# Performance work log

Hardware: AMD Instinct MI355X
Metric: run time of the kernel (lower is better)

## Reference

```python
import jax, jax.numpy as jnp
import numpy as np

B, C, H, W, N = 256, 64, 36, 36, 2000
P = H * W  # 1296 mask pixels


def setup_inputs() -> dict:
    key = jax.random.key(0)
    k1, k2, k3 = jax.random.split(key, 3)
    x = jax.random.normal(k1, (B, C, H, W), dtype=jnp.float32)
    # init_scales rows 1 and 2 give (mean=0, std=0.01) for both param tensors
    mask_weights = 0.01 * jax.random.normal(k2, (P, C, N), dtype=jnp.float32)
    readout_weights = 0.01 * jax.random.normal(k3, (C, N), dtype=jnp.float32)
    return {"x": x, "mask_weights": mask_weights, "readout_weights": readout_weights}


def reference(x, mask_weights, readout_weights):
    # x: (B, C, H, W) -> flatten spatial dims to P
    b, c, h, w = x.shape
    x_flat = x.reshape(b, c, h * w)  # (B, C, P)
    # Per-channel spatial pooling fused with weighted channel sum:
    # masked[b,c,n] = sum_p x_flat[b,c,p] * mask_weights[p,c,n]
    # out[b,n]     = sum_c masked[b,c,n] * readout_weights[c,n]
    out = jnp.einsum("bcp,pcn,cn->bn", x_flat, mask_weights, readout_weights)
    # final_relu=False => no bias / softplus
    return out
```

## Files before the change

kernel.cpp:

```cpp
#include <hip/hip_runtime.h>

typedef unsigned short ushort_t;
typedef unsigned int uint_t;
typedef __attribute__((ext_vector_type(8))) short bf16x8;
typedef __attribute__((ext_vector_type(4))) float f32x4;

#define C_DIM 64
#define P_DIM 1296
#define N_DIM 2000
#define B_DIM 256
#define K_DIM (C_DIM * P_DIM)
#define XB_ELEMS (B_DIM * K_DIM)
#define XB_ELEMS_PAD (XB_ELEMS + 256)
#define XB_BYTES ((size_t)XB_ELEMS_PAD * 2)
#define SLICES 32
#define OUT_ELEMS (B_DIM * N_DIM)
#define NSTEP 42

static __device__ __forceinline__ ushort_t f2bf(float f) {
  unsigned u = __builtin_bit_cast(unsigned, f);
  u += 0x7fffu + ((u >> 16) & 1u);
  return (ushort_t)(u >> 16);
}

__global__ void klindt_cvt_kernel(const float4* __restrict__ x,
                                  unsigned long long* __restrict__ xb) {
  int idx = blockIdx.x * 256 + threadIdx.x;
  if (idx >= XB_ELEMS_PAD / 4) return;
  unsigned long long r = 0ull;
  if (idx < XB_ELEMS / 4) {
    float4 v = x[idx];
    r = (unsigned long long)f2bf(v.x) | ((unsigned long long)f2bf(v.y) << 16) |
        ((unsigned long long)f2bf(v.z) << 32) |
        ((unsigned long long)f2bf(v.w) << 48);
  }
  xb[idx] = r;
}

__global__ void __launch_bounds__(512, 4) klindt_gemm_kernel(
    const char* __restrict__ xbb, const char* __restrict__ mwb,
    const float* __restrict__ rw, float* __restrict__ partials) {
  __shared__ ushort_t sA[2][16384];

  const int tid = threadIdx.x;
  const int lane = tid & 63;
  const int wid = tid >> 6;
  const int r15 = lane & 15, g4 = lane >> 4;
  const int bid = blockIdx.x;
  const int slice = (bid & 7) + 8 * ((bid >> 3) & 3);
  const int n0 = (bid >> 5) * 128;
  const int c0 = slice * 2;

  f32x4 acc[16];
#pragma unroll
  for (int i = 0; i < 16; ++i) {
    acc[i][0] = 0.f; acc[i][1] = 0.f; acc[i][2] = 0.f; acc[i][3] = 0.f;
  }

  uint_t a_gbase[4]; int a_doff[4];
#pragma unroll
  for (int it = 0; it < 4; ++it) {
    int chunk = it * 512 + tid;
    int row = chunk >> 3, sl = chunk & 7;
    int ss = sl ^ (row & 7);
    a_gbase[it] = (uint_t)(row * K_DIM + ss * 8) * 2u;
    a_doff[it] = chunk * 8;
  }

  const int nidx = n0 + wid * 16 + r15;
  const bool okn = nidx < N_DIM;
  const uint_t nb4 = (uint_t)(okn ? nidx : (N_DIM - 1)) * 4u;
  const float rvl = okn ? rw[c0 * N_DIM + nidx] : 0.f;
  const float rvh = okn ? rw[(c0 + 1) * N_DIM + nidx] : 0.f;
  const uint_t pg = (uint_t)(g4 * 8);

  const int swz7 = r15 & 7;
  const int aoff0 = r15 * 128 + ((g4 ^ swz7) & 7) * 16;
  const int aoff1 = r15 * 128 + (((g4 + 4) ^ swz7) & 7) * 16;

  float mvE[16], mvO[16];

  auto issueA = [&](int buf, int t) {
    int half = (t >= 21) ? 1 : 0;
    int sp = t - 21 * half;
    uint_t kb = ((uint_t)(c0 + half) * (uint_t)P_DIM + (uint_t)sp * 64u) * 2u;
#pragma unroll
    for (int it = 0; it < 4; ++it) {
      const char* g = xbb + (a_gbase[it] + kb);
      __builtin_amdgcn_global_load_lds(
          (const __attribute__((address_space(1))) unsigned int*)g,
          (__attribute__((address_space(3))) unsigned int*)(&sA[buf][a_doff[it]]),
          16, 0, 0);
    }
  };

#define ISSUE_B(MV, T)                                                        \
  do {                                                                        \
    int half_ = ((T) >= 21) ? 1 : 0;                                          \
    int sp_ = (T)-21 * half_;                                                 \
    uint_t pa_ = (uint_t)(sp_ * 64) + pg;                                     \
    uint_t pb_ = pa_ + 32u;                                                   \
    if (pa_ > 1288u) pa_ = 1288u;       \
    if (pb_ > 1288u) pb_ = 1288u;                                             \
    uint_t cb_ = (uint_t)(c0 + half_) * 8000u + nb4;                          \
    const char* ba_ = mwb + (pa_ * 512000u + cb_);                            \
    const char* bb_ = mwb + (pb_ * 512000u + cb_);                            \
    _Pragma("unroll") for (int j_ = 0; j_ < 8; ++j_)                          \
        MV[j_] = *(const float*)(ba_ + (uint_t)j_ * 512000u);                 \
    _Pragma("unroll") for (int j_ = 0; j_ < 8; ++j_)                          \
        MV[8 + j_] = *(const float*)(bb_ + (uint_t)j_ * 512000u);             \
  } while (0)

#define CVT_COMPUTE(BUF, MV, T)                                               \
  do {                                                                        \
    int half_ = ((T) >= 21) ? 1 : 0;                                          \
    int sp_ = (T)-21 * half_;                                                 \
    float rv_ = half_ ? rvh : rvl;                                            \
    float rva_ = (sp_ < 20 || g4 < 2) ? rv_ : 0.f;                            \
    float rvb_ = (sp_ < 20) ? rv_ : 0.f;                                      \
    bf16x8 b0_, b1_;                                                          \
    _Pragma("unroll") for (int j_ = 0; j_ < 8; ++j_) {                        \
      b0_[j_] = (short)f2bf(MV[j_] * rva_);                                   \
      b1_[j_] = (short)f2bf(MV[8 + j_] * rvb_);                               \
    }                                                                         \
    __builtin_amdgcn_s_setprio(1);                                            \
    _Pragma("unroll") for (int fm_ = 0; fm_ < 16; ++fm_) {                    \
      bf16x8 a0_ = *(const bf16x8*)((const char*)&sA[BUF][0] +                \
                                    (aoff0 + fm_ * 2048));                    \
      acc[fm_] = __builtin_amdgcn_mfma_f32_16x16x32_bf16(a0_, b0_, acc[fm_],  \
                                                         0, 0, 0);            \
      bf16x8 a1_ = *(const bf16x8*)((const char*)&sA[BUF][0] +                \
                                    (aoff1 + fm_ * 2048));                    \
      acc[fm_] = __builtin_amdgcn_mfma_f32_16x16x32_bf16(a1_, b1_, acc[fm_],  \
                                                         0, 0, 0);            \
    }                                                                         \
    __builtin_amdgcn_s_setprio(0);                                            \
  } while (0)

  issueA(0, 0);
  ISSUE_B(mvE, 0);
  asm volatile("s_waitcnt vmcnt(16) lgkmcnt(0)" ::: "memory");
  __builtin_amdgcn_sched_barrier(0);
  __builtin_amdgcn_s_barrier();
  __builtin_amdgcn_sched_barrier(0);

#define BODY(S, MV_CUR, MV_NEXT)                                              \
  {                                                                           \
    issueA(((S) + 1) & 1, (S) + 1);            \
    ISSUE_B(MV_NEXT, (S) + 1);             \
    CVT_COMPUTE((S)&1, MV_CUR, S);        \
    asm volatile("s_waitcnt vmcnt(16) lgkmcnt(0)" ::: "memory");              \
    __builtin_amdgcn_sched_barrier(0);                                        \
    __builtin_amdgcn_s_barrier();                                             \
    __builtin_amdgcn_sched_barrier(0);                                        \
  }

  for (int s = 0; s < 40; s += 2) {
    BODY(s, mvE, mvO);
    BODY(s + 1, mvO, mvE);
  }
  BODY(40, mvE, mvO);
  CVT_COMPUTE(1, mvO, 41);

  float* pb = partials + (size_t)slice * OUT_ELEMS;
  if (okn) {
#pragma unroll
    for (int fm = 0; fm < 16; ++fm) {
#pragma unroll
      for (int rr = 0; rr < 4; ++rr) {
        int m = fm * 16 + g4 * 4 + rr;
        pb[m * N_DIM + nidx] = acc[fm][rr];
      }
    }
  }
#undef BODY
#undef ISSUE_B
#undef CVT_COMPUTE
}

__global__ void klindt_reduce_kernel(const float* __restrict__ part,
                                     float* __restrict__ out) {
  int i = blockIdx.x * 256 + threadIdx.x;
  if (i < OUT_ELEMS) {
    float s = 0.f;
#pragma unroll
    for (int k = 0; k < SLICES; ++k) s += part[(size_t)k * OUT_ELEMS + i];
    out[i] = s;
  }
}

extern "C" void kernel_launch(void* const* d_in, const int* in_sizes, int n_in,
                              void* d_out, int out_size, void* d_ws,
                              size_t ws_size, hipStream_t stream) {
  (void)in_sizes; (void)n_in; (void)out_size; (void)ws_size;
  const float* x = (const float*)d_in[0];
  const char* mwb = (const char*)d_in[1];
  const float* rw = (const float*)d_in[2];
  float* out = (float*)d_out;

  char* xbb = (char*)d_ws;
  float* partials = (float*)((char*)d_ws + XB_BYTES);

  {
    int nvec = XB_ELEMS_PAD / 4;
    int grid = (nvec + 255) / 256;
    klindt_cvt_kernel<<<grid, 256, 0, stream>>>((const float4*)x,
                                                (unsigned long long*)xbb);
  }
  {
    klindt_gemm_kernel<<<512, 512, 0, stream>>>(xbb, mwb, rw, partials);
  }
  {
    int grid = (OUT_ELEMS + 255) / 256;
    klindt_reduce_kernel<<<grid, 256, 0, stream>>>(partials, out);
  }
}
```

Baseline: 244.8 us.

## Retile GEMM to per-wave private LDS buffers with 128x32 wave tiles, no block barriers

The GEMM kernel changes from 512-thread blocks covering all 256 batch rows and 128 outputs to 256-thread blocks covering 128 rows. Each wave stages its own A tile in a private LDS region and computes a 128x32 output tile. This drops the block-wide s_barrier per K step and halves A reuse across waves, so each wave issues 16 LDS-direct loads per step. The aim is to remove block synchronization stalls and raise occupancy. The cost is more redundant A traffic from global/L2 and single-buffered staging within each wave.

```diff
diff --git a/kernel.cpp b/kernel.cpp
--- a/kernel.cpp
+++ b/kernel.cpp
@@ -15,7 +15,6 @@
 #define XB_BYTES ((size_t)XB_ELEMS_PAD * 2)
 #define SLICES 32
 #define OUT_ELEMS (B_DIM * N_DIM)
-#define NSTEP 42
 
 static __device__ __forceinline__ ushort_t f2bf(float f) {
   unsigned u = __builtin_bit_cast(unsigned, f);
@@ -37,10 +36,10 @@
   xb[idx] = r;
 }
 
-__global__ void __launch_bounds__(512, 4) klindt_gemm_kernel(
+__global__ void __launch_bounds__(256, 2) klindt_gemm_kernel(
     const char* __restrict__ xbb, const char* __restrict__ mwb,
     const float* __restrict__ rw, float* __restrict__ partials) {
-  __shared__ ushort_t sA[2][16384];
+  __shared__ ushort_t sA[4][8192];
 
   const int tid = threadIdx.x;
   const int lane = tid & 63;
@@ -48,134 +47,149 @@
   const int r15 = lane & 15, g4 = lane >> 4;
   const int bid = blockIdx.x;
   const int slice = (bid & 7) + 8 * ((bid >> 3) & 3);
-  const int n0 = (bid >> 5) * 128;
+  const int r5 = bid >> 5;
+  const int m0 = (r5 & 1) * 128;
+  const int nb = ((r5 >> 1) * 4 + wid) * 32;
   const int c0 = slice * 2;
 
-  f32x4 acc[16];
-#pragma unroll
-  for (int i = 0; i < 16; ++i) {
-    acc[i][0] = 0.f; acc[i][1] = 0.f; acc[i][2] = 0.f; acc[i][3] = 0.f;
-  }
-
-  uint_t a_gbase[4]; int a_doff[4];
-#pragma unroll
-  for (int it = 0; it < 4; ++it) {
-    int chunk = it * 512 + tid;
-    int row = chunk >> 3, sl = chunk & 7;
-    int ss = sl ^ (row & 7);
-    a_gbase[it] = (uint_t)(row * K_DIM + ss * 8) * 2u;
-    a_doff[it] = chunk * 8;
-  }
-
-  const int nidx = n0 + wid * 16 + r15;
-  const bool okn = nidx < N_DIM;
-  const uint_t nb4 = (uint_t)(okn ? nidx : (N_DIM - 1)) * 4u;
-  const float rvl = okn ? rw[c0 * N_DIM + nidx] : 0.f;
-  const float rvh = okn ? rw[(c0 + 1) * N_DIM + nidx] : 0.f;
+  ushort_t* myA = sA[wid];
+
+  f32x4 acc[8][2];
+#pragma unroll
+  for (int i = 0; i < 8; ++i)
+#pragma unroll
+    for (int j = 0; j < 2; ++j) {
+      acc[i][j][0] = 0.f; acc[i][j][1] = 0.f;
+      acc[i][j][2] = 0.f; acc[i][j][3] = 0.f;
+    }
+
+  const int ss8 = (((lane & 7) ^ ((lane >> 3) & 7))) * 8;
+  const uint_t a_srcm = (uint_t)(m0 + (lane >> 3)) * (uint_t)K_DIM * 2u;
+
+  const int nA = nb + r15, nB = nb + 16 + r15;
+  const bool okA = nA < N_DIM, okB = nB < N_DIM;
+  const uint_t nAb = (uint_t)(okA ? nA : N_DIM - 1) * 4u;
+  const uint_t nBb = (uint_t)(okB ? nB : N_DIM - 1) * 4u;
+  const float rv0l = okA ? rw[c0 * N_DIM + nA] : 0.f;
+  const float rv1l = okB ? rw[c0 * N_DIM + nB] : 0.f;
+  const float rv0h = okA ? rw[(c0 + 1) * N_DIM + nA] : 0.f;
+  const float rv1h = okB ? rw[(c0 + 1) * N_DIM + nB] : 0.f;
   const uint_t pg = (uint_t)(g4 * 8);
 
-  const int swz7 = r15 & 7;
-  const int aoff0 = r15 * 128 + ((g4 ^ swz7) & 7) * 16;
-  const int aoff1 = r15 * 128 + (((g4 + 4) ^ swz7) & 7) * 16;
+  const int aoff0 = r15 * 128 + ((g4 ^ (r15 & 7)) & 7) * 16;
+  const int aoff1 = r15 * 128 + (((g4 + 4) ^ (r15 & 7)) & 7) * 16;
 
   float mvE[16], mvO[16];
-
-  auto issueA = [&](int buf, int t) {
-    int half = (t >= 21) ? 1 : 0;
-    int sp = t - 21 * half;
-    uint_t kb = ((uint_t)(c0 + half) * (uint_t)P_DIM + (uint_t)sp * 64u) * 2u;
-#pragma unroll
-    for (int it = 0; it < 4; ++it) {
-      const char* g = xbb + (a_gbase[it] + kb);
-      __builtin_amdgcn_global_load_lds(
-          (const __attribute__((address_space(1))) unsigned int*)g,
-          (__attribute__((address_space(3))) unsigned int*)(&sA[buf][a_doff[it]]),
-          16, 0, 0);
+  bf16x8 bf0, bf1;
+
+#define STAGE(C, P0)                                                          \
+  do {                                                                        \
+    uint_t kl_ = (uint_t)(P0) + (uint_t)ss8;                                  \
+    if (kl_ > 1288u) kl_ = 1288u;                \
+    uint_t ko_ = ((uint_t)(C) * (uint_t)P_DIM + kl_) * 2u;                    \
+    const char* s_ = xbb + (a_srcm + ko_);                                    \
+    _Pragma("unroll") for (int i_ = 0; i_ < 16; ++i_)                         \
+        __builtin_amdgcn_global_load_lds(                                     \
+            (const __attribute__((address_space(1))) unsigned int*)           \
+                (s_ + i_ * 1327104),                                          \
+            (__attribute__((address_space(3))) unsigned int*)(&myA[i_ * 512]),\
+            16, 0, 0);                                                        \
+  } while (0)
+
+#define ISSUE_B(MV, C_, SP_)                                                  \
+  do {                                                                        \
+    uint_t ps_ = (uint_t)((SP_)*32) + pg;                                     \
+    if (ps_ > 1288u) ps_ = 1288u;                                             \
+    const char* base_ = mwb + (ps_ * 512000u + (uint_t)(C_)*8000u);           \
+    _Pragma("unroll") for (int j_ = 0; j_ < 8; ++j_) {                        \
+      MV[j_] = *(const float*)(base_ + (uint_t)j_ * 512000u + nAb);           \
+      MV[8 + j_] = *(const float*)(base_ + (uint_t)j_ * 512000u + nBb);       \
+    }                                                                         \
+  } while (0)
+
+#define CVT(MV, RA, RB, TAIL)                                                 \
+  do {                                                                        \
+    float ra_ = (RA), rb_ = (RB);                                             \
+    if ((TAIL) && g4 >= 2) { ra_ = 0.f; rb_ = 0.f; }                          \
+    _Pragma("unroll") for (int j_ = 0; j_ < 8; ++j_) {                        \
+      bf0[j_] = (short)f2bf(MV[j_] * ra_);                                    \
+      bf1[j_] = (short)f2bf(MV[8 + j_] * rb_);                                \
+    }                                                                         \
+  } while (0)
+
+#define MFMA_STEP(AOFF)                                                       \
+  do {                                                                        \
+    __builtin_amdgcn_s_setprio(1);                                            \
+    _Pragma("unroll") for (int fm_ = 0; fm_ < 8; ++fm_) {                     \
+      bf16x8 a_ = *(const bf16x8*)((const char*)myA + ((AOFF) + fm_ * 2048)); \
+      acc[fm_][0] =                                                           \
+          __builtin_amdgcn_mfma_f32_16x16x32_bf16(a_, bf0, acc[fm_][0], 0,0,0);\
+      acc[fm_][1] =                                                           \
+          __builtin_amdgcn_mfma_f32_16x16x32_bf16(a_, bf1, acc[fm_][1], 0,0,0);\
+    }                                                                         \
+    __builtin_amdgcn_s_setprio(0);                                            \
+  } while (0)
+
+#define GUARD                                                                 \
+  asm volatile("s_waitcnt lgkmcnt(0)" ::: "memory");                          \
+  __builtin_amdgcn_sched_barrier(0)
+#define VM16                                                                  \
+  asm volatile("s_waitcnt vmcnt(16)" ::: "memory");                           \
+  __builtin_amdgcn_sched_barrier(0)
+#define VM0                                                                   \
+  asm volatile("s_waitcnt vmcnt(0)" ::: "memory");                            \
+  __builtin_amdgcn_sched_barrier(0)
+
+#define CHANNEL(C, MVA, MVB, RA, RB, LASTCH)                                  \
+  do {                                                                        \
+    for (int u_ = 0; u_ < 20; ++u_) {                                         \
+      GUARD;                                                                  \
+      STAGE(C, u_ * 64);                                                      \
+      __builtin_amdgcn_sched_barrier(0);                                      \
+      ISSUE_B(MVB, C, 2 * u_ + 1);                                            \
+      CVT(MVA, RA, RB, false);                                                \
+      VM16;                                                                   \
+      MFMA_STEP(aoff0);                                                       \
+      ISSUE_B(MVA, C, 2 * u_ + 2);           \
+      CVT(MVB, RA, RB, false);                                                \
+      MFMA_STEP(aoff1);                                                       \
+    }                                                                         \
+    GUARD;                                                                    \
+    STAGE(C, 1280);                                                           \
+    __builtin_amdgcn_sched_barrier(0);                                        \
+    if (!(LASTCH)) { ISSUE_B(MVB, (C) + 1, 0); }                              \
+    CVT(MVA, RA, RB, true);                                                   \
+    if (LASTCH) { VM0; } else { VM16; }                                       \
+    MFMA_STEP(aoff0);                                                         \
+  } while (0)
+
+  ISSUE_B(mvE, c0, 0);
+  CHANNEL(c0, mvE, mvO, rv0l, rv1l, false);
+  CHANNEL(c0 + 1, mvO, mvE, rv0h, rv1h, true);
+
+  float* pb = partials + (size_t)slice * OUT_ELEMS;
+#pragma unroll
+  for (int fm = 0; fm < 8; ++fm) {
+    int m = m0 + fm * 16 + g4 * 4;
+    if (okA) {
+#pragma unroll
+      for (int rr = 0; rr < 4; ++rr)
+        pb[(m + rr) * N_DIM + nA] = acc[fm][0][rr];
     }
-  };
-
-#define ISSUE_B(MV, T)                                                        \
-  do {                                                                        \
-    int half_ = ((T) >= 21) ? 1 : 0;                                          \
-    int sp_ = (T)-21 * half_;                                                 \
-    uint_t pa_ = (uint_t)(sp_ * 64) + pg;                                     \
-    uint_t pb_ = pa_ + 32u;                                                   \
-    if (pa_ > 1288u) pa_ = 1288u;       \
-    if (pb_ > 1288u) pb_ = 1288u;                                             \
-    uint_t cb_ = (uint_t)(c0 + half_) * 8000u + nb4;                          \
-    const char* ba_ = mwb + (pa_ * 512000u + cb_);                            \
-    const char* bb_ = mwb + (pb_ * 512000u + cb_);                            \
-    _Pragma("unroll") for (int j_ = 0; j_ < 8; ++j_)                          \
-        MV[j_] = *(const float*)(ba_ + (uint_t)j_ * 512000u);                 \
-    _Pragma("unroll") for (int j_ = 0; j_ < 8; ++j_)                          \
-        MV[8 + j_] = *(const float*)(bb_ + (uint_t)j_ * 512000u);             \
-  } while (0)
-
-#define CVT_COMPUTE(BUF, MV, T)                                               \
-  do {                                                                        \
-    int half_ = ((T) >= 21) ? 1 : 0;                                          \
-    int sp_ = (T)-21 * half_;                                                 \
-    float rv_ = half_ ? rvh : rvl;                                            \
-    float rva_ = (sp_ < 20 || g4 < 2) ? rv_ : 0.f;                            \
-    float rvb_ = (sp_ < 20) ? rv_ : 0.f;                                      \
-    bf16x8 b0_, b1_;                                                          \
-    _Pragma("unroll") for (int j_ = 0; j_ < 8; ++j_) {                        \
-      b0_[j_] = (short)f2bf(MV[j_] * rva_);                                   \
-      b1_[j_] = (short)f2bf(MV[8 + j_] * rvb_);                               \
-    }                                                                         \
-    __builtin_amdgcn_s_setprio(1);                                            \
-    _Pragma("unroll") for (int fm_ = 0; fm_ < 16; ++fm_) {                    \
-      bf16x8 a0_ = *(const bf16x8*)((const char*)&sA[BUF][0] +                \
-                                    (aoff0 + fm_ * 2048));                    \
-      acc[fm_] = __builtin_amdgcn_mfma_f32_16x16x32_bf16(a0_, b0_, acc[fm_],  \
-                                                         0, 0, 0);            \
-      bf16x8 a1_ = *(const bf16x8*)((const char*)&sA[BUF][0] +                \
-                                    (aoff1 + fm_ * 2048));                    \
-      acc[fm_] = __builtin_amdgcn_mfma_f32_16x16x32_bf16(a1_, b1_, acc[fm_],  \
-                                                         0, 0, 0);            \
-    }                                                                         \
-    __builtin_amdgcn_s_setprio(0);                                            \
-  } while (0)
-
-  issueA(0, 0);
-  ISSUE_B(mvE, 0);
-  asm volatile("s_waitcnt vmcnt(16) lgkmcnt(0)" ::: "memory");
-  __builtin_amdgcn_sched_barrier(0);
-  __builtin_amdgcn_s_barrier();
-  __builtin_amdgcn_sched_barrier(0);
-
-#define BODY(S, MV_CUR, MV_NEXT)                                              \
-  {                                                                           \
-    issueA(((S) + 1) & 1, (S) + 1);            \
-    ISSUE_B(MV_NEXT, (S) + 1);             \
-    CVT_COMPUTE((S)&1, MV_CUR, S);        \
-    asm volatile("s_waitcnt vmcnt(16) lgkmcnt(0)" ::: "memory");              \
-    __builtin_amdgcn_sched_barrier(0);                                        \
-    __builtin_amdgcn_s_barrier();                                             \
-    __builtin_amdgcn_sched_barrier(0);                                        \
-  }
-
-  for (int s = 0; s < 40; s += 2) {
-    BODY(s, mvE, mvO);
-    BODY(s + 1, mvO, mvE);
-  }
-  BODY(40, mvE, mvO);
-  CVT_COMPUTE(1, mvO, 41);
-
-  float* pb = partials + (size_t)slice * OUT_ELEMS;
-  if (okn) {
-#pragma unroll
-    for (int fm = 0; fm < 16; ++fm) {
-#pragma unroll
-      for (int rr = 0; rr < 4; ++rr) {
-        int m = fm * 16 + g4 * 4 + rr;
-        pb[m * N_DIM + nidx] = acc[fm][rr];
-      }
+    if (okB) {
+#pragma unroll
+      for (int rr = 0; rr < 4; ++rr)
+        pb[(m + rr) * N_DIM + nB] = acc[fm][1][rr];
     }
   }
-#undef BODY
+#undef CHANNEL
+#undef VM0
+#undef VM16
+#undef GUARD
+#undef MFMA_STEP
+#undef CVT
 #undef ISSUE_B
-#undef CVT_COMPUTE
+#undef STAGE
 }
 
 __global__ void klindt_reduce_kernel(const float* __restrict__ part,
@@ -208,7 +222,7 @@
                                                 (unsigned long long*)xbb);
   }
   {
-    klindt_gemm_kernel<<<512, 512, 0, stream>>>(xbb, mwb, rw, partials);
+    klindt_gemm_kernel<<<1024, 256, 0, stream>>>(xbb, mwb, rw, partials);
   }
   {
     int grid = (OUT_ELEMS + 255) / 256;
```

After: 388.9 us. 58.8% more time.
